# Kernel tuning notes

Measured on AMD Instinct MI355X. Metric: run time of the kernel, lower is better.

The kernel has to match this reference:

```python
import jax, jax.numpy as jnp
import numpy as np
import math

HIDDEN = 1024
HEADS = 16
HEAD_DIM = HIDDEN // HEADS
RANK = 16
LORA_SCALING = 1.0 / RANK  # loralib default lora_alpha=1 -> scaling = alpha/r


def setup_inputs() -> dict:
    key = jax.random.key(0)
    ks = jax.random.split(key, 16)
    bs, seq = 4, 2048
    inp = {
        "hidden_states": jax.random.normal(ks[0], (bs, seq, HIDDEN), dtype=jnp.float32),
        "attention_mask": jnp.zeros((bs, 1, 1, seq), dtype=jnp.float32),
    }
    s = 0.02
    for i, nm in enumerate(["q", "k", "v"]):
        inp[f"W{nm}"] = jax.random.normal(ks[1 + 4 * i], (HIDDEN, HIDDEN), dtype=jnp.float32) * s
        inp[f"b{nm}"] = jnp.zeros((HIDDEN,), dtype=jnp.float32)
        inp[f"A{nm}"] = jax.random.normal(ks[2 + 4 * i], (RANK, HIDDEN), dtype=jnp.float32) * s
        inp[f"B{nm}"] = jnp.zeros((HIDDEN, RANK), dtype=jnp.float32)  # loralib inits B to zero
    return inp


def _lora_linear(x, W, b, A, B):
    # y = x W^T + b + scaling * (x A^T) B^T
    return x @ W.T + b + LORA_SCALING * ((x @ A.T) @ B.T)


def _transform(x, W, b, A, B, bs, seq):
    proj = _lora_linear(x, W, b, A, B)  # [bs, seq, hidden]
    return proj.reshape(bs, seq, HEADS, HEAD_DIM).transpose(0, 2, 1, 3)  # [bs, h, seq, d]


def reference(hidden_states, attention_mask, Wq, bq, Aq, Bq, Wk, bk, Ak, Bk, Wv, bv, Av, Bv):
    bs, seq, _ = hidden_states.shape
    q = _transform(hidden_states, Wq, bq, Aq, Bq, bs, seq)
    k = _transform(hidden_states, Wk, bk, Ak, Bk, bs, seq)
    v = _transform(hidden_states, Wv, bv, Av, Bv, bs, seq)
    scores = jnp.einsum("bhqd,bhkd->bhqk", q, k) / math.sqrt(HEAD_DIM) + attention_mask
    probs = jax.nn.softmax(scores, axis=-1)  # [bs, h, seq, seq]
    out = jnp.einsum("bhqk,bhkd->bhqd", probs, v)  # [bs, h, seq, d]
    return out.transpose(0, 2, 1, 3).reshape(bs, seq, HIDDEN)
```

## Files before the change

### kernel.cpp

```cpp
#include <hip/hip_runtime.h>
#include <stdint.h>

typedef __bf16 bf16x8 __attribute__((ext_vector_type(8)));
typedef float f32x4 __attribute__((ext_vector_type(4)));
typedef float f32x16 __attribute__((ext_vector_type(16)));
typedef short s16x4 __attribute__((ext_vector_type(4)));

#define HAS_X8 __has_builtin(__builtin_amdgcn_mfma_f32_32x32x8bf16_1k)

static __device__ __forceinline__ unsigned short f2bf(float f) {
  unsigned int x = __float_as_uint(f);
  unsigned int r = (x + 0x7fffu + ((x >> 16) & 1u)) >> 16;
  return (unsigned short)r;
}
static __device__ __forceinline__ unsigned int pk_bf16(float a, float b) {
  unsigned int d;
  asm("v_cvt_pk_bf16_f32 %0, %1, %2" : "=v"(d) : "v"(a), "v"(b));
  return d;
}
static __device__ __forceinline__ float exp2_hw(float x) {
  float r;
  asm("v_exp_f32 %0, %1" : "=v"(r) : "v"(x));
  return r;
}
static __device__ __forceinline__ float rcp_hw(float x) {
  float r;
  asm("v_rcp_f32 %0, %1" : "=v"(r) : "v"(x));
  return r;
}
static __device__ __forceinline__ void gll16(const void* g, void* l) {
  __builtin_amdgcn_global_load_lds((const __attribute__((address_space(1))) unsigned int*)g,
                                   (__attribute__((address_space(3))) unsigned int*)l,
                                   16, 0, 0);
}

__global__ __launch_bounds__(256) void convert_x(const float* __restrict__ X,
                                                 unsigned short* __restrict__ Xbf) {
  int i = (blockIdx.x * 256 + threadIdx.x) * 4;
  float4 v = *(const float4*)(X + i);
  uint2 o;
  o.x = pk_bf16(v.x, v.y);
  o.y = pk_bf16(v.z, v.w);
  *(uint2*)(Xbf + i) = o;
}

__global__ __launch_bounds__(256) void build_weff(
    const float* __restrict__ Wq, const float* __restrict__ Aq, const float* __restrict__ Bq,
    const float* __restrict__ Wk, const float* __restrict__ Ak, const float* __restrict__ Bk,
    const float* __restrict__ Wv, const float* __restrict__ Av, const float* __restrict__ Bv,
    unsigned short* __restrict__ Weff) {
  int idx = blockIdx.x * 256 + threadIdx.x;
  int p = idx >> 20;
  int o = (idx >> 10) & 1023;
  int i = idx & 1023;
  const float* W = (p == 0) ? Wq : (p == 1) ? Wk : Wv;
  const float* A = (p == 0) ? Aq : (p == 1) ? Ak : Av;
  const float* B = (p == 0) ? Bq : (p == 1) ? Bk : Bv;
  float acc = 0.f;
#pragma unroll
  for (int r = 0; r < 16; ++r)
    acc += B[o * 16 + r] * A[r * 1024 + i];
  Weff[idx] = f2bf(W[o * 1024 + i] + acc * 0.0625f);
}

__global__ __launch_bounds__(256) void gemm_qkv(
    const unsigned short* __restrict__ X, const unsigned short* __restrict__ Weff,
    const float* __restrict__ bq, const float* __restrict__ bk, const float* __restrict__ bv,
    unsigned short* __restrict__ qbuf, unsigned short* __restrict__ kbuf,
    unsigned short* __restrict__ vtbuf) {
  __shared__ __align__(16) unsigned short As[128][64];
  __shared__ __align__(16) unsigned short Bs[128][64];
  const int K = 1024;
  int tid = threadIdx.x;
  int lane = tid & 63;
  int w = tid >> 6;
  int wm = (w >> 1) * 64;
  int wn = (w & 1) * 64;
  int c = lane & 15;
  int quad = lane >> 4;

  int bid = blockIdx.x;
  int grp = bid / 192;
  int rem = bid % 192;
  int m0 = (grp * 8 + (rem & 7)) * 128;
  int n0 = (rem >> 3) * 128;
  int p = n0 >> 10;

  int ldr = lane >> 3;
  int ldc = (lane & 7) * 8;
  const unsigned short* gA = X + (m0 + w * 32 + ldr) * K + ldc;
  const unsigned short* gB = Weff + (n0 + w * 32 + ldr) * K + ldc;

  f32x4 acc[4][4] = {};

  if (p == 2) {
    for (int k0 = 0; k0 < K; k0 += 64) {
      __syncthreads();
#pragma unroll
      for (int i = 0; i < 4; i++) {
        gll16(gA + k0 + i * 8 * K, &As[w * 32 + i * 8][0]);
        gll16(gB + k0 + i * 8 * K, &Bs[w * 32 + i * 8][0]);
      }
      __syncthreads();
#pragma unroll
      for (int kk = 0; kk < 64; kk += 32) {
        bf16x8 af[4], bfr[4];
#pragma unroll
        for (int mi = 0; mi < 4; mi++)
          af[mi] = *(const bf16x8*)&As[wm + mi * 16 + c][kk + quad * 8];
#pragma unroll
        for (int ni = 0; ni < 4; ni++)
          bfr[ni] = *(const bf16x8*)&Bs[wn + ni * 16 + c][kk + quad * 8];
#pragma unroll
        for (int mi = 0; mi < 4; mi++)
#pragma unroll
          for (int ni = 0; ni < 4; ni++)
            acc[mi][ni] = __builtin_amdgcn_mfma_f32_16x16x32_bf16(af[mi], bfr[ni], acc[mi][ni], 0, 0, 0);
      }
    }
    const float* bias = bv;
#pragma unroll
    for (int ni = 0; ni < 4; ni++) {
      int o = (n0 + wn + ni * 16 + c) & 1023;
      int h = o >> 6;
      int d = o & 63;
      float bval = bias[o];
#pragma unroll
      for (int mi = 0; mi < 4; mi++) {
        int mbase = m0 + wm + mi * 16 + quad * 4;
        int bb = mbase >> 11;
        int s = mbase & 2047;
        uint2 o4;
        o4.x = pk_bf16(acc[mi][ni][0] + bval, acc[mi][ni][1] + bval);
        o4.y = pk_bf16(acc[mi][ni][2] + bval, acc[mi][ni][3] + bval);
        *(uint2*)&vtbuf[((bb * 16 + h) * 64 + d) * 2048 + s] = o4;
      }
    }
  } else {
    for (int k0 = 0; k0 < K; k0 += 64) {
      __syncthreads();
#pragma unroll
      for (int i = 0; i < 4; i++) {
        gll16(gA + k0 + i * 8 * K, &As[w * 32 + i * 8][0]);
        gll16(gB + k0 + i * 8 * K, &Bs[w * 32 + i * 8][0]);
      }
      __syncthreads();
#pragma unroll
      for (int kk = 0; kk < 64; kk += 32) {
        bf16x8 af[4], bfr[4];
#pragma unroll
        for (int mi = 0; mi < 4; mi++)
          af[mi] = *(const bf16x8*)&As[wm + mi * 16 + c][kk + quad * 8];
#pragma unroll
        for (int ni = 0; ni < 4; ni++)
          bfr[ni] = *(const bf16x8*)&Bs[wn + ni * 16 + c][kk + quad * 8];
#pragma unroll
        for (int mi = 0; mi < 4; mi++)
#pragma unroll
          for (int ni = 0; ni < 4; ni++)
            acc[mi][ni] = __builtin_amdgcn_mfma_f32_16x16x32_bf16(bfr[ni], af[mi], acc[mi][ni], 0, 0, 0);
      }
    }
    const float* bias = (p == 1) ? bk : bq;
    unsigned short* dst = (p == 1) ? kbuf : qbuf;
#pragma unroll
    for (int mi = 0; mi < 4; mi++) {
      int m = m0 + wm + mi * 16 + c;
      int bb = m >> 11;
      int ss = m & 2047;
#pragma unroll
      for (int ni = 0; ni < 4; ni++) {
        int o = (n0 + wn + ni * 16 + quad * 4) & 1023;
        int h = o >> 6;
        int d = o & 63;
        float4 b4 = *(const float4*)&bias[o];
        uint2 o4;
        o4.x = pk_bf16(acc[mi][ni][0] + b4.x, acc[mi][ni][1] + b4.y);
        o4.y = pk_bf16(acc[mi][ni][2] + b4.z, acc[mi][ni][3] + b4.w);
        *(uint2*)&dst[((bb * 16 + h) * 2048 + ss) * 64 + d] = o4;
      }
    }
  }
}

__global__ __launch_bounds__(256, 2) void attn_kernel(
    const unsigned short* __restrict__ qbuf, const unsigned short* __restrict__ kbuf,
    const unsigned short* __restrict__ vtbuf, const float* __restrict__ maskg,
    float* __restrict__ out) {
  __shared__ __align__(16) unsigned short Ks[64][72];
  __shared__ __align__(16) unsigned short Vts[64][72];
  __shared__ __align__(16) float masks2[2048];
  __shared__ __align__(16) float lrow[256];

  const float SC = 0.125f * 1.4426950408889634f;
  const float L2E = 1.4426950408889634f;

  int tid = threadIdx.x;
  int lane = tid & 63;
  int w = tid >> 6;
  int m31 = lane & 31;
  int hi = lane >> 5;
  int bh = blockIdx.y;
  int b = bh >> 4;
  int h = bh & 15;
  int q0 = blockIdx.x * 256;

  const unsigned short* Qbh = qbuf + bh * (2048 * 64);
  const unsigned short* Kbh = kbuf + bh * (2048 * 64);
  const unsigned short* Vbh = vtbuf + bh * (64 * 2048);

#pragma unroll
  for (int i = 0; i < 2; i++) {
    int idx = (i * 256 + tid) * 4;
    float4 mm = *(const float4*)(maskg + b * 2048 + idx);
    float4 mo;
    mo.x = (mm.x - 8.f) * L2E;
    mo.y = (mm.y - 8.f) * L2E;
    mo.z = (mm.z - 8.f) * L2E;
    mo.w = (mm.w - 8.f) * L2E;
    *(float4*)&masks2[idx] = mo;
  }

  bf16x8 qfr[2][4];
#pragma unroll
  for (int qb = 0; qb < 2; qb++)
#pragma unroll
    for (int ks = 0; ks < 4; ks++)
      qfr[qb][ks] = *(const bf16x8*)(Qbh + (q0 + w * 64 + qb * 32 + m31) * 64 + ks * 16 + hi * 8);

  int r2 = tid >> 3;
  int ch = (tid & 7) * 8;

  uint4 pkv0 = *(const uint4*)(Kbh + r2 * 64 + ch);
  uint4 pkv1 = *(const uint4*)(Kbh + (32 + r2) * 64 + ch);
  uint4 pkv2 = *(const uint4*)(Vbh + r2 * 2048 + ch);
  uint4 pkv3 = *(const uint4*)(Vbh + (r2 + 32) * 2048 + ch);

  float lsum[2] = {0.f, 0.f};
  f32x16 acc_o[2][2] = {};

  for (int kt = 0; kt < 2048; kt += 64) {
    __syncthreads();
    *(uint4*)&Ks[r2][ch] = pkv0;
    *(uint4*)&Ks[r2 + 32][ch] = pkv1;
    *(uint4*)&Vts[r2][ch] = pkv2;
    *(uint4*)&Vts[r2 + 32][ch] = pkv3;
    __syncthreads();
    int kn = (kt + 64) & 2047;
    pkv0 = *(const uint4*)(Kbh + (kn + r2) * 64 + ch);
    pkv1 = *(const uint4*)(Kbh + (kn + 32 + r2) * 64 + ch);
    pkv2 = *(const uint4*)(Vbh + r2 * 2048 + kn + ch);
    pkv3 = *(const uint4*)(Vbh + (r2 + 32) * 2048 + kn + ch);

#pragma unroll
    for (int kb = 0; kb < 2; kb++) {
      f32x16 accs[2] = {};
#pragma unroll
      for (int ks = 0; ks < 4; ks++) {
        bf16x8 kf = *(const bf16x8*)&Ks[kb * 32 + m31][ks * 16 + hi * 8];
#pragma unroll
        for (int qb = 0; qb < 2; qb++)
          accs[qb] = __builtin_amdgcn_mfma_f32_32x32x16_bf16(kf, qfr[qb][ks], accs[qb], 0, 0, 0);
      }

      unsigned int up[2][4][2];
#pragma unroll
      for (int g = 0; g < 4; g++) {
        float4 m4 = *(const float4*)&masks2[kt + kb * 32 + g * 8 + hi * 4];
#pragma unroll
        for (int qb = 0; qb < 2; qb++) {
          float p0 = exp2_hw(fmaf(accs[qb][g * 4 + 0], SC, m4.x));
          float p1 = exp2_hw(fmaf(accs[qb][g * 4 + 1], SC, m4.y));
          float p2 = exp2_hw(fmaf(accs[qb][g * 4 + 2], SC, m4.z));
          float p3 = exp2_hw(fmaf(accs[qb][g * 4 + 3], SC, m4.w));
          lsum[qb] += (p0 + p1) + (p2 + p3);
          up[qb][g][0] = pk_bf16(p0, p1);
          up[qb][g][1] = pk_bf16(p2, p3);
        }
      }

#if HAS_X8
#pragma unroll
      for (int g = 0; g < 4; g++) {
        int col = kb * 32 + g * 8 + hi * 4;
#pragma unroll
        for (int db = 0; db < 2; db++) {
          union { uint2 u; s16x4 s; } vc;
          vc.u = *(const uint2*)&Vts[db * 32 + m31][col];
#pragma unroll
          for (int qb = 0; qb < 2; qb++) {
            union { uint2 u; s16x4 s; } pc;
            pc.u.x = up[qb][g][0];
            pc.u.y = up[qb][g][1];
            acc_o[db][qb] = __builtin_amdgcn_mfma_f32_32x32x8bf16_1k(pc.s, vc.s, acc_o[db][qb], 0, 0, 0);
          }
        }
      }
#else
#pragma unroll
      for (int gp = 0; gp < 2; gp++) {
        union { uint4 u; bf16x8 bv8; } pf[2];
#pragma unroll
        for (int qb = 0; qb < 2; qb++) {
          unsigned int A0 = up[qb][gp * 2][0], A1 = up[qb][gp * 2][1];
          unsigned int B0 = up[qb][gp * 2 + 1][0], B1 = up[qb][gp * 2 + 1][1];
          unsigned int A0x = (unsigned int)__shfl_xor((int)A0, 32);
          unsigned int A1x = (unsigned int)__shfl_xor((int)A1, 32);
          unsigned int B0x = (unsigned int)__shfl_xor((int)B0, 32);
          unsigned int B1x = (unsigned int)__shfl_xor((int)B1, 32);
          pf[qb].u.x = hi ? B0x : A0;
          pf[qb].u.y = hi ? B1x : A1;
          pf[qb].u.z = hi ? B0 : A0x;
          pf[qb].u.w = hi ? B1 : A1x;
        }
#pragma unroll
        for (int db = 0; db < 2; db++) {
          bf16x8 vf = *(const bf16x8*)&Vts[db * 32 + m31][kb * 32 + gp * 16 + hi * 8];
#pragma unroll
          for (int qb = 0; qb < 2; qb++)
            acc_o[db][qb] = __builtin_amdgcn_mfma_f32_32x32x16_bf16(pf[qb].bv8, vf, acc_o[db][qb], 0, 0, 0);
        }
      }
#endif
    }
  }

#pragma unroll
  for (int qb = 0; qb < 2; qb++) {
    lsum[qb] += __shfl_xor(lsum[qb], 32);
    lrow[w * 64 + qb * 32 + m31] = lsum[qb];
  }
  __asm__ volatile("" ::: "memory");

#pragma unroll
  for (int qb = 0; qb < 2; qb++)
#pragma unroll
    for (int g = 0; g < 4; g++) {
      float4 l4 = *(const float4*)&lrow[w * 64 + qb * 32 + g * 8 + hi * 4];
      float i0 = rcp_hw(l4.x), i1 = rcp_hw(l4.y), i2 = rcp_hw(l4.z), i3 = rcp_hw(l4.w);
      int qq = q0 + w * 64 + qb * 32 + g * 8 + hi * 4;
#pragma unroll
      for (int db = 0; db < 2; db++) {
        float* obase = out + (b * 2048 + qq) * 1024 + h * 64 + db * 32 + m31;
        obase[0 * 1024] = acc_o[db][qb][g * 4 + 0] * i0;
        obase[1 * 1024] = acc_o[db][qb][g * 4 + 1] * i1;
        obase[2 * 1024] = acc_o[db][qb][g * 4 + 2] * i2;
        obase[3 * 1024] = acc_o[db][qb][g * 4 + 3] * i3;
      }
    }
}

extern "C" void kernel_launch(void* const* d_in, const int* in_sizes, int n_in,
                              void* d_out, int out_size, void* d_ws, size_t ws_size,
                              hipStream_t stream) {
  const float* X    = (const float*)d_in[0];
  const float* mask = (const float*)d_in[1];
  const float* Wq = (const float*)d_in[2];
  const float* bq = (const float*)d_in[3];
  const float* Aq = (const float*)d_in[4];
  const float* Bq = (const float*)d_in[5];
  const float* Wk = (const float*)d_in[6];
  const float* bk = (const float*)d_in[7];
  const float* Ak = (const float*)d_in[8];
  const float* Bk = (const float*)d_in[9];
  const float* Wv = (const float*)d_in[10];
  const float* bv = (const float*)d_in[11];
  const float* Av = (const float*)d_in[12];
  const float* Bv = (const float*)d_in[13];

  unsigned short* ws    = (unsigned short*)d_ws;
  unsigned short* Xbf   = ws;
  unsigned short* Weff  = Xbf + 8388608;
  unsigned short* qbuf  = Weff + 3145728;
  unsigned short* kbuf  = qbuf + 8388608;
  unsigned short* vtbuf = kbuf + 8388608;

  convert_x<<<dim3(8192), dim3(256), 0, stream>>>(X, Xbf);
  build_weff<<<dim3(12288), dim3(256), 0, stream>>>(Wq, Aq, Bq, Wk, Ak, Bk, Wv, Av, Bv, Weff);
  gemm_qkv<<<dim3(1536), dim3(256), 0, stream>>>(Xbf, Weff, bq, bk, bv, qbuf, kbuf, vtbuf);
  attn_kernel<<<dim3(8, 64), dim3(256), 0, stream>>>(qbuf, kbuf, vtbuf, mask, (float*)d_out);
}
```

Before: 286.1 us.

## Double-buffer K/V tiles in attention, remap grid, vectorize weight build

The attention kernel now double-buffers its K and V shared tiles. This drops one of the two barriers per key tile, and the next tile is written into the alternate buffer after compute. The grid becomes 1D with a remapping that groups blocks sharing a (batch, head) set so K/V reuse in L2 is better. build_weff processes four elements per thread with float4 loads and packed bf16 stores. Shared memory use roughly doubles for K/V, which may affect the occupancy of two blocks per CU.

```diff
diff --git a/kernel.cpp b/kernel.cpp
--- a/kernel.cpp
+++ b/kernel.cpp
@@ -49,18 +49,26 @@
     const float* __restrict__ Wk, const float* __restrict__ Ak, const float* __restrict__ Bk,
     const float* __restrict__ Wv, const float* __restrict__ Av, const float* __restrict__ Bv,
     unsigned short* __restrict__ Weff) {
-  int idx = blockIdx.x * 256 + threadIdx.x;
+  int idx = (blockIdx.x * 256 + threadIdx.x) * 4;
   int p = idx >> 20;
   int o = (idx >> 10) & 1023;
   int i = idx & 1023;
   const float* W = (p == 0) ? Wq : (p == 1) ? Wk : Wv;
   const float* A = (p == 0) ? Aq : (p == 1) ? Ak : Av;
   const float* B = (p == 0) ? Bq : (p == 1) ? Bk : Bv;
-  float acc = 0.f;
-#pragma unroll
-  for (int r = 0; r < 16; ++r)
-    acc += B[o * 16 + r] * A[r * 1024 + i];
-  Weff[idx] = f2bf(W[o * 1024 + i] + acc * 0.0625f);
+  float4 acc = {0.f, 0.f, 0.f, 0.f};
+#pragma unroll
+  for (int r = 0; r < 16; ++r) {
+    float bb = B[o * 16 + r];
+    float4 av = *(const float4*)&A[r * 1024 + i];
+    acc.x += bb * av.x; acc.y += bb * av.y;
+    acc.z += bb * av.z; acc.w += bb * av.w;
+  }
+  float4 wv = *(const float4*)&W[o * 1024 + i];
+  uint2 ov;
+  ov.x = pk_bf16(wv.x + acc.x * 0.0625f, wv.y + acc.y * 0.0625f);
+  ov.y = pk_bf16(wv.z + acc.z * 0.0625f, wv.w + acc.w * 0.0625f);
+  *(uint2*)&Weff[idx] = ov;
 }
 
 __global__ __launch_bounds__(256) void gemm_qkv(
@@ -187,8 +195,8 @@
     const unsigned short* __restrict__ qbuf, const unsigned short* __restrict__ kbuf,
     const unsigned short* __restrict__ vtbuf, const float* __restrict__ maskg,
     float* __restrict__ out) {
-  __shared__ __align__(16) unsigned short Ks[64][72];
-  __shared__ __align__(16) unsigned short Vts[64][72];
+  __shared__ __align__(16) unsigned short Ks[2][64][72];
+  __shared__ __align__(16) unsigned short Vts[2][64][72];
   __shared__ __align__(16) float masks2[2048];
   __shared__ __align__(16) float lrow[256];
 
@@ -200,10 +208,13 @@
   int w = tid >> 6;
   int m31 = lane & 31;
   int hi = lane >> 5;
-  int bh = blockIdx.y;
+
+  int g = blockIdx.x;
+  int qt = (g >> 3) & 7;
+  int bh = ((g >> 6) << 3) | (g & 7);
   int b = bh >> 4;
   int h = bh & 15;
-  int q0 = blockIdx.x * 256;
+  int q0 = qt * 256;
 
   const unsigned short* Qbh = qbuf + bh * (2048 * 64);
   const unsigned short* Kbh = kbuf + bh * (2048 * 64);
@@ -231,33 +242,36 @@
   int r2 = tid >> 3;
   int ch = (tid & 7) * 8;
 
-  uint4 pkv0 = *(const uint4*)(Kbh + r2 * 64 + ch);
-  uint4 pkv1 = *(const uint4*)(Kbh + (32 + r2) * 64 + ch);
-  uint4 pkv2 = *(const uint4*)(Vbh + r2 * 2048 + ch);
-  uint4 pkv3 = *(const uint4*)(Vbh + (r2 + 32) * 2048 + ch);
+  {
+    uint4 t0 = *(const uint4*)(Kbh + r2 * 64 + ch);
+    uint4 t1 = *(const uint4*)(Kbh + (32 + r2) * 64 + ch);
+    uint4 t2 = *(const uint4*)(Vbh + r2 * 2048 + ch);
+    uint4 t3 = *(const uint4*)(Vbh + (r2 + 32) * 2048 + ch);
+    *(uint4*)&Ks[0][r2][ch] = t0;
+    *(uint4*)&Ks[0][r2 + 32][ch] = t1;
+    *(uint4*)&Vts[0][r2][ch] = t2;
+    *(uint4*)&Vts[0][r2 + 32][ch] = t3;
+  }
+  uint4 pkv0 = *(const uint4*)(Kbh + (64 + r2) * 64 + ch);
+  uint4 pkv1 = *(const uint4*)(Kbh + (64 + 32 + r2) * 64 + ch);
+  uint4 pkv2 = *(const uint4*)(Vbh + r2 * 2048 + 64 + ch);
+  uint4 pkv3 = *(const uint4*)(Vbh + (r2 + 32) * 2048 + 64 + ch);
+
+  __syncthreads();
 
   float lsum[2] = {0.f, 0.f};
   f32x16 acc_o[2][2] = {};
 
-  for (int kt = 0; kt < 2048; kt += 64) {
-    __syncthreads();
-    *(uint4*)&Ks[r2][ch] = pkv0;
-    *(uint4*)&Ks[r2 + 32][ch] = pkv1;
-    *(uint4*)&Vts[r2][ch] = pkv2;
-    *(uint4*)&Vts[r2 + 32][ch] = pkv3;
-    __syncthreads();
-    int kn = (kt + 64) & 2047;
-    pkv0 = *(const uint4*)(Kbh + (kn + r2) * 64 + ch);
-    pkv1 = *(const uint4*)(Kbh + (kn + 32 + r2) * 64 + ch);
-    pkv2 = *(const uint4*)(Vbh + r2 * 2048 + kn + ch);
-    pkv3 = *(const uint4*)(Vbh + (r2 + 32) * 2048 + kn + ch);
+  for (int t = 0; t < 32; t++) {
+    int cur = t & 1;
+    int kt = t * 64;
 
 #pragma unroll
     for (int kb = 0; kb < 2; kb++) {
       f32x16 accs[2] = {};
 #pragma unroll
       for (int ks = 0; ks < 4; ks++) {
-        bf16x8 kf = *(const bf16x8*)&Ks[kb * 32 + m31][ks * 16 + hi * 8];
+        bf16x8 kf = *(const bf16x8*)&Ks[cur][kb * 32 + m31][ks * 16 + hi * 8];
 #pragma unroll
         for (int qb = 0; qb < 2; qb++)
           accs[qb] = __builtin_amdgcn_mfma_f32_32x32x16_bf16(kf, qfr[qb][ks], accs[qb], 0, 0, 0);
@@ -265,33 +279,33 @@
 
       unsigned int up[2][4][2];
 #pragma unroll
-      for (int g = 0; g < 4; g++) {
-        float4 m4 = *(const float4*)&masks2[kt + kb * 32 + g * 8 + hi * 4];
+      for (int gg = 0; gg < 4; gg++) {
+        float4 m4 = *(const float4*)&masks2[kt + kb * 32 + gg * 8 + hi * 4];
 #pragma unroll
         for (int qb = 0; qb < 2; qb++) {
-          float p0 = exp2_hw(fmaf(accs[qb][g * 4 + 0], SC, m4.x));
-          float p1 = exp2_hw(fmaf(accs[qb][g * 4 + 1], SC, m4.y));
-          float p2 = exp2_hw(fmaf(accs[qb][g * 4 + 2], SC, m4.z));
-          float p3 = exp2_hw(fmaf(accs[qb][g * 4 + 3], SC, m4.w));
+          float p0 = exp2_hw(fmaf(accs[qb][gg * 4 + 0], SC, m4.x));
+          float p1 = exp2_hw(fmaf(accs[qb][gg * 4 + 1], SC, m4.y));
+          float p2 = exp2_hw(fmaf(accs[qb][gg * 4 + 2], SC, m4.z));
+          float p3 = exp2_hw(fmaf(accs[qb][gg * 4 + 3], SC, m4.w));
           lsum[qb] += (p0 + p1) + (p2 + p3);
-          up[qb][g][0] = pk_bf16(p0, p1);
-          up[qb][g][1] = pk_bf16(p2, p3);
+          up[qb][gg][0] = pk_bf16(p0, p1);
+          up[qb][gg][1] = pk_bf16(p2, p3);
         }
       }
 
 #if HAS_X8
 #pragma unroll
-      for (int g = 0; g < 4; g++) {
-        int col = kb * 32 + g * 8 + hi * 4;
+      for (int gg = 0; gg < 4; gg++) {
+        int col = kb * 32 + gg * 8 + hi * 4;
 #pragma unroll
         for (int db = 0; db < 2; db++) {
           union { uint2 u; s16x4 s; } vc;
-          vc.u = *(const uint2*)&Vts[db * 32 + m31][col];
+          vc.u = *(const uint2*)&Vts[cur][db * 32 + m31][col];
 #pragma unroll
           for (int qb = 0; qb < 2; qb++) {
             union { uint2 u; s16x4 s; } pc;
-            pc.u.x = up[qb][g][0];
-            pc.u.y = up[qb][g][1];
+            pc.u.x = up[qb][gg][0];
+            pc.u.y = up[qb][gg][1];
             acc_o[db][qb] = __builtin_amdgcn_mfma_f32_32x32x8bf16_1k(pc.s, vc.s, acc_o[db][qb], 0, 0, 0);
           }
         }
@@ -315,7 +329,7 @@
         }
 #pragma unroll
         for (int db = 0; db < 2; db++) {
-          bf16x8 vf = *(const bf16x8*)&Vts[db * 32 + m31][kb * 32 + gp * 16 + hi * 8];
+          bf16x8 vf = *(const bf16x8*)&Vts[cur][db * 32 + m31][kb * 32 + gp * 16 + hi * 8];
 #pragma unroll
           for (int qb = 0; qb < 2; qb++)
             acc_o[db][qb] = __builtin_amdgcn_mfma_f32_32x32x16_bf16(pf[qb].bv8, vf, acc_o[db][qb], 0, 0, 0);
@@ -323,6 +337,20 @@
       }
 #endif
     }
+
+    if (t < 31) {
+      int nb = cur ^ 1;
+      *(uint4*)&Ks[nb][r2][ch] = pkv0;
+      *(uint4*)&Ks[nb][r2 + 32][ch] = pkv1;
+      *(uint4*)&Vts[nb][r2][ch] = pkv2;
+      *(uint4*)&Vts[nb][r2 + 32][ch] = pkv3;
+      int kn = (kt + 128) & 2047;
+      pkv0 = *(const uint4*)(Kbh + (kn + r2) * 64 + ch);
+      pkv1 = *(const uint4*)(Kbh + (kn + 32 + r2) * 64 + ch);
+      pkv2 = *(const uint4*)(Vbh + r2 * 2048 + kn + ch);
+      pkv3 = *(const uint4*)(Vbh + (r2 + 32) * 2048 + kn + ch);
+    }
+    __syncthreads();
   }
 
 #pragma unroll
@@ -335,17 +363,17 @@
 #pragma unroll
   for (int qb = 0; qb < 2; qb++)
 #pragma unroll
-    for (int g = 0; g < 4; g++) {
-      float4 l4 = *(const float4*)&lrow[w * 64 + qb * 32 + g * 8 + hi * 4];
+    for (int gg = 0; gg < 4; gg++) {
+      float4 l4 = *(const float4*)&lrow[w * 64 + qb * 32 + gg * 8 + hi * 4];
       float i0 = rcp_hw(l4.x), i1 = rcp_hw(l4.y), i2 = rcp_hw(l4.z), i3 = rcp_hw(l4.w);
-      int qq = q0 + w * 64 + qb * 32 + g * 8 + hi * 4;
+      int qq = q0 + w * 64 + qb * 32 + gg * 8 + hi * 4;
 #pragma unroll
       for (int db = 0; db < 2; db++) {
         float* obase = out + (b * 2048 + qq) * 1024 + h * 64 + db * 32 + m31;
-        obase[0 * 1024] = acc_o[db][qb][g * 4 + 0] * i0;
-        obase[1 * 1024] = acc_o[db][qb][g * 4 + 1] * i1;
-        obase[2 * 1024] = acc_o[db][qb][g * 4 + 2] * i2;
-        obase[3 * 1024] = acc_o[db][qb][g * 4 + 3] * i3;
+        obase[0 * 1024] = acc_o[db][qb][gg * 4 + 0] * i0;
+        obase[1 * 1024] = acc_o[db][qb][gg * 4 + 1] * i1;
+        obase[2 * 1024] = acc_o[db][qb][gg * 4 + 2] * i2;
+        obase[3 * 1024] = acc_o[db][qb][gg * 4 + 3] * i3;
       }
     }
 }
@@ -376,7 +404,7 @@
   unsigned short* vtbuf = kbuf + 8388608;
 
   convert_x<<<dim3(8192), dim3(256), 0, stream>>>(X, Xbf);
-  build_weff<<<dim3(12288), dim3(256), 0, stream>>>(Wq, Aq, Bq, Wk, Ak, Bk, Wv, Av, Bv, Weff);
+  build_weff<<<dim3(3072), dim3(256), 0, stream>>>(Wq, Aq, Bq, Wk, Ak, Bk, Wv, Av, Bv, Weff);
   gemm_qkv<<<dim3(1536), dim3(256), 0, stream>>>(Xbf, Weff, bq, bk, bv, qbuf, kbuf, vtbuf);
-  attn_kernel<<<dim3(8, 64), dim3(256), 0, stream>>>(qbuf, kbuf, vtbuf, mask, (float*)d_out);
-}
+  attn_kernel<<<dim3(512), dim3(256), 0, stream>>>(qbuf, kbuf, vtbuf, mask, (float*)d_out);
+}
```

Measured after the change: 278.0 us. 1.03x faster.
